# Kernel optimization log

Measured on AMD Instinct MI355X. Metric: run time of the kernel, lower is better.

Reference implementation:

```python
import jax, jax.numpy as jnp
import numpy as np

N = 100000       # nodes
E = 1200000      # edges
D_IN = 64
D_OUT = 64
ALPHA = 0.01     # LeakyReLU negative slope
EPS = 1e-5       # BatchNorm eps


def setup_inputs() -> dict:
    key = jax.random.key(0)
    k0, k1, k2, k3 = jax.random.split(key, 4)
    x = jax.random.normal(k0, (N, D_IN), dtype=jnp.float32)
    edge_idx = jax.random.randint(k1, (2, E), 0, N)
    edge_attr = jax.random.uniform(k2, (E,), dtype=jnp.float32)
    W = jax.random.normal(k3, (D_IN, D_OUT), dtype=jnp.float32) * (1.0 / np.sqrt(D_IN))
    b = jnp.zeros((D_OUT,), dtype=jnp.float32)
    gamma = jnp.ones((D_OUT,), dtype=jnp.float32)
    beta = jnp.zeros((D_OUT,), dtype=jnp.float32)
    return {"x": x, "edge_idx": edge_idx, "edge_attr": edge_attr,
            "W": W, "b": b, "gamma": gamma, "beta": beta}


def reference(x, edge_idx, edge_attr, W, b, gamma, beta):
    n = x.shape[0]
    row, col = edge_idx[0], edge_idx[1]
    # --- GCNConv: add self-loops, symmetric normalization ---
    loops = jnp.arange(n)
    row_f = jnp.concatenate([row, loops])                       # [E+N]
    col_f = jnp.concatenate([col, loops])                       # [E+N]
    w_f = jnp.concatenate([edge_attr, jnp.ones((n,), x.dtype)])  # [E+N]
    deg = jax.ops.segment_sum(w_f, col_f, num_segments=n)       # [N]
    deg_safe = jnp.where(deg > 0, deg, 1.0)
    dis = jnp.where(deg > 0, jax.lax.rsqrt(deg_safe), 0.0)      # deg^-1/2
    norm = dis[row_f] * w_f * dis[col_f]                        # [E+N]
    h = x @ W                                                   # [N, D_OUT]
    msg = norm[:, None] * h[row_f]                              # gather + scale
    agg = jax.ops.segment_sum(msg, col_f, num_segments=n) + b   # scatter-add
    # --- BatchNorm (training-mode batch stats, biased var) ---
    mean = jnp.mean(agg, axis=0)
    var = jnp.mean((agg - mean) ** 2, axis=0)
    hn = (agg - mean) * jax.lax.rsqrt(var + EPS) * gamma + beta
    # --- LeakyReLU ---
    return jnp.where(hn >= 0, hn, ALPHA * hn)
```

## Files before the change

kernel.cpp:

```cpp
#include <hip/hip_runtime.h>

#define D 64
#define ALPHA 0.01f
#define EPS 1e-5f
#define NREP 8
#define CAP 48
#define GSZ 128
#define GMAX 1024
#define NB 512
#define CHUNK 2368
#define BT 512

typedef __attribute__((ext_vector_type(8))) short short8;
typedef __attribute__((ext_vector_type(4))) float f32x4;

__device__ inline unsigned short f2bf(float f) {
    unsigned u = __float_as_uint(f);
    u += 0x7fffu + ((u >> 16) & 1u);
    return (unsigned short)(u >> 16);
}
__device__ inline float bf2f(unsigned short h) { return __uint_as_float((unsigned)h << 16); }

__global__ __launch_bounds__(BT) void k_prepbin(const float4* __restrict__ x4,
                                                ushort4* __restrict__ xb4,
                                                float* __restrict__ stats,
                                                const int* __restrict__ eidx,
                                                const float* __restrict__ w,
                                                uint2* __restrict__ seg,
                                                unsigned short* __restrict__ off16,
                                                long long n16, int G, int E, int chunk) {
    __shared__ uint2 rec[CHUNK];
    __shared__ int h[GMAX + 2];
    __shared__ int ls[BT];
    if (blockIdx.x < NB) {
        int b = blockIdx.x, t = threadIdx.x;
        int e0 = b * chunk;
        int e1 = e0 + chunk; if (e1 > E) e1 = E;
        for (int i = t; i < GMAX + 2; i += BT) h[i] = 0;
        __syncthreads();
        for (int e = e0 + t; e < e1; e += BT) {
            int row = eidx[e];
            int c = eidx[E + e];
            unsigned wq = (unsigned)(w[e] * 32767.0f + 0.5f);
            rec[e - e0] = make_uint2((wq << 17) | (unsigned)row, (unsigned)c);
            atomicAdd(&h[c >> 7], 1);
        }
        __syncthreads();
        int i0 = 2 * t, i1 = 2 * t + 1;
        int a0 = h[i0];
        int a1 = h[i1];
        ls[t] = a0 + a1;
        __syncthreads();
        int own = ls[t];
        for (int off = 1; off < BT; off <<= 1) {
            int v = (t >= off) ? ls[t - off] : 0;
            __syncthreads();
            ls[t] += v;
            __syncthreads();
        }
        int excl = ls[t] - own;
        __syncthreads();
        h[i0] = excl;
        h[i1] = excl + a0;
        __syncthreads();
        unsigned short* ob = off16 + (size_t)b * (G + 1);
        for (int g = t; g <= G; g += BT) ob[g] = (unsigned short)h[g];
        __syncthreads();
        for (int e = e0 + t; e < e1; e += BT) {
            uint2 rv = rec[e - e0];
            int c = (int)rv.y;
            int slot = atomicAdd(&h[c >> 7], 1);
            seg[e0 + slot] = make_uint2(rv.x, (unsigned)(c & (GSZ - 1)));
        }
    } else {
        long long i = (long long)(blockIdx.x - NB) * BT + threadIdx.x;
        if (i < n16) {
            float4 v = x4[i];
            ushort4 r;
            r.x = f2bf(v.x); r.y = f2bf(v.y); r.z = f2bf(v.z); r.w = f2bf(v.w);
            xb4[i] = r;
        }
        if (i < NREP * 128) stats[i] = 0.0f;
    }
}

__global__ __launch_bounds__(BT) void k_binC2(const uint2* __restrict__ seg,
                                              const unsigned short* __restrict__ off16,
                                              unsigned* __restrict__ bucket,
                                              int* __restrict__ cnt,
                                              float* __restrict__ dis,
                                              float* __restrict__ dis_s,
                                              int G, int chunk, int n) {
    __shared__ int cl[GSZ];
    __shared__ float ws[GSZ];
    int g = blockIdx.x;
    if (threadIdx.x < GSZ) { cl[threadIdx.x] = 0; ws[threadIdx.x] = 0.0f; }
    __syncthreads();
    int b = threadIdx.x;
    const unsigned short* ob = off16 + (size_t)b * (G + 1);
    int s = ob[g], e = ob[g + 1];
    size_t base = (size_t)b * chunk;
    for (int i = s; i < e; ++i) {
        uint2 ev = seg[base + i];
        int cig = (int)ev.y;
        int rank = atomicAdd(&cl[cig], 1);
        atomicAdd(&ws[cig], (float)(ev.x >> 17) * (1.0f / 32767.0f));
        int node = g * GSZ + cig;
        if (rank < CAP) bucket[(size_t)node * CAP + rank] = ev.x;
    }
    __syncthreads();
    if (threadIdx.x < GSZ) {
        int node = g * GSZ + threadIdx.x;
        if (node < n) {
            cnt[node] = cl[threadIdx.x];
            float d = rsqrtf(1.0f + ws[threadIdx.x]);
            dis[node] = d;
            dis_s[node] = d * (1.0f / 32767.0f);
        }
    }
}

__global__ __launch_bounds__(256) void k_gather(const unsigned short* __restrict__ xb,
                                                const unsigned* __restrict__ bucket,
                                                const int* __restrict__ cnt,
                                                const float* __restrict__ dis,
                                                const float* __restrict__ dis_s,
                                                unsigned short* __restrict__ aggb, int n) {
    int node = blockIdx.x * 4 + (threadIdx.x >> 6);
    if (node >= n) return;
    int lane = threadIdx.x & 63;
    int g = lane >> 3;
    int l = lane & 7;
    int c = cnt[node];
    if (c > CAP) c = CAP;
    float di = dis[node];
    float acc[8] = {0, 0, 0, 0, 0, 0, 0, 0};
    if (g == 0) {
        short8 xv = *(const short8*)(xb + ((size_t)node << 6) + l * 8);
#pragma unroll
        for (int k = 0; k < 8; ++k) acc[k] = bf2f((unsigned short)xv[k]) * di;
    }
    const unsigned* bkt = bucket + (size_t)node * CAP;
    int j0 = g, j1 = g + 8;
    unsigned v0 = (j0 < c) ? bkt[j0] : 0u;
    unsigned v1 = (j1 < c) ? bkt[j1] : 0u;
    while (j0 < c) {
        int p0 = j0 + 16, p1 = j1 + 16;
        unsigned w0 = (p0 < c) ? bkt[p0] : 0u;
        unsigned w1 = (p1 < c) ? bkt[p1] : 0u;
        int s0 = (int)(v0 & 0x1FFFFu);
        int s1 = (int)(v1 & 0x1FFFFu);
        float nr0 = (float)(v0 >> 17) * dis_s[s0];
        float nr1 = (float)(v1 >> 17) * dis_s[s1];
        short8 x0 = *(const short8*)(xb + ((size_t)s0 << 6) + l * 8);
        short8 x1 = *(const short8*)(xb + ((size_t)s1 << 6) + l * 8);
#pragma unroll
        for (int k = 0; k < 8; ++k) acc[k] += nr0 * bf2f((unsigned short)x0[k]);
#pragma unroll
        for (int k = 0; k < 8; ++k) acc[k] += nr1 * bf2f((unsigned short)x1[k]);
        v0 = w0; v1 = w1; j0 = p0; j1 = p1;
    }
#pragma unroll
    for (int off = 8; off <= 32; off <<= 1)
#pragma unroll
        for (int k = 0; k < 8; ++k) acc[k] += __shfl_xor(acc[k], off, 64);
    if (g == 0) {
        short8 r;
#pragma unroll
        for (int k = 0; k < 8; ++k) r[k] = (short)f2bf(acc[k] * di);
        *(short8*)(aggb + ((size_t)node << 6) + l * 8) = r;
    }
}

__global__ __launch_bounds__(256) void k_gemmstats(const unsigned short* __restrict__ aggb,
                                                   const float* __restrict__ Wm,
                                                   float* __restrict__ stats, int n) {
    __shared__ unsigned short Wt[64 * 64];
    __shared__ float ssum[4][64], qsum[4][64];
    int tid = threadIdx.x;
    for (int i = tid; i < 4096; i += 256) {
        int k = i >> 6, nn = i & 63;
        Wt[nn * 64 + k] = f2bf(Wm[i]);
    }
    __syncthreads();
    int wv = tid >> 6;
    int lane = tid & 63;
    int l15 = lane & 15;
    int quad = lane >> 4;

    short8 bfrag[2][4];
#pragma unroll
    for (int h = 0; h < 2; ++h)
#pragma unroll
        for (int g = 0; g < 4; ++g)
            bfrag[h][g] = *(const short8*)&Wt[(g * 16 + l15) * 64 + h * 32 + quad * 8];

    float s[4] = {0, 0, 0, 0}, q[4] = {0, 0, 0, 0};
    int nwt = (n + 15) >> 4;
    for (int wt = blockIdx.x * 4 + wv; wt < nwt; wt += gridDim.x * 4) {
        int row0 = wt * 16;
        int arow = row0 + l15;
        if (arow >= n) arow = n - 1;
        const unsigned short* ap = aggb + (size_t)arow * 64 + quad * 8;
        short8 a0 = *(const short8*)ap;
        short8 a1 = *(const short8*)(ap + 32);
        f32x4 acc[4] = {{0, 0, 0, 0}, {0, 0, 0, 0}, {0, 0, 0, 0}, {0, 0, 0, 0}};
#pragma unroll
        for (int g = 0; g < 4; ++g) {
            acc[g] = __builtin_amdgcn_mfma_f32_16x16x32_bf16(a0, bfrag[0][g], acc[g], 0, 0, 0);
            acc[g] = __builtin_amdgcn_mfma_f32_16x16x32_bf16(a1, bfrag[1][g], acc[g], 0, 0, 0);
        }
#pragma unroll
        for (int r = 0; r < 4; ++r) {
            int row = row0 + quad * 4 + r;
            if (row < n) {
#pragma unroll
                for (int g = 0; g < 4; ++g) {
                    float v = acc[g][r];
                    s[g] += v;
                    q[g] += v * v;
                }
            }
        }
    }
#pragma unroll
    for (int off = 16; off <= 32; off <<= 1) {
#pragma unroll
        for (int g = 0; g < 4; ++g) {
            s[g] += __shfl_xor(s[g], off, 64);
            q[g] += __shfl_xor(q[g], off, 64);
        }
    }
    if (quad == 0) {
#pragma unroll
        for (int g = 0; g < 4; ++g) { ssum[wv][g * 16 + l15] = s[g]; qsum[wv][g * 16 + l15] = q[g]; }
    }
    __syncthreads();
    float* st = stats + (blockIdx.x & (NREP - 1)) * 128;
    if (tid < 64)
        atomicAdd(&st[tid], ssum[0][tid] + ssum[1][tid] + ssum[2][tid] + ssum[3][tid]);
    else if (tid < 128) {
        int t = tid - 64;
        atomicAdd(&st[64 + t], qsum[0][t] + qsum[1][t] + qsum[2][t] + qsum[3][t]);
    }
}

__global__ __launch_bounds__(256) void k_gemmbn(const unsigned short* __restrict__ aggb,
                                                const float* __restrict__ Wm,
                                                float* __restrict__ out,
                                                const float* __restrict__ stats,
                                                const float* __restrict__ gamma,
                                                const float* __restrict__ beta, int n) {
    __shared__ unsigned short Wt[64 * 64];
    __shared__ float scale[64], shift[64];
    int tid = threadIdx.x;
    for (int i = tid; i < 4096; i += 256) {
        int k = i >> 6, nn = i & 63;
        Wt[nn * 64 + k] = f2bf(Wm[i]);
    }
    if (tid < 64) {
        float sm = 0.0f, qm = 0.0f;
#pragma unroll
        for (int r = 0; r < NREP; ++r) {
            sm += stats[r * 128 + tid];
            qm += stats[r * 128 + 64 + tid];
        }
        float inv_n = 1.0f / (float)n;
        float mean = sm * inv_n;
        float var = qm * inv_n - mean * mean;
        float sc = rsqrtf(var + EPS) * gamma[tid];
        scale[tid] = sc;
        shift[tid] = beta[tid] - mean * sc;
    }
    __syncthreads();
    int wv = tid >> 6;
    int lane = tid & 63;
    int l15 = lane & 15;
    int quad = lane >> 4;

    short8 bfrag[2][4];
    float bsc[4], bsh[4];
#pragma unroll
    for (int h = 0; h < 2; ++h)
#pragma unroll
        for (int g = 0; g < 4; ++g)
            bfrag[h][g] = *(const short8*)&Wt[(g * 16 + l15) * 64 + h * 32 + quad * 8];
#pragma unroll
    for (int g = 0; g < 4; ++g) { bsc[g] = scale[g * 16 + l15]; bsh[g] = shift[g * 16 + l15]; }

    int nwt = (n + 15) >> 4;
    for (int wt = blockIdx.x * 4 + wv; wt < nwt; wt += gridDim.x * 4) {
        int row0 = wt * 16;
        int arow = row0 + l15;
        if (arow >= n) arow = n - 1;
        const unsigned short* ap = aggb + (size_t)arow * 64 + quad * 8;
        short8 a0 = *(const short8*)ap;
        short8 a1 = *(const short8*)(ap + 32);
        f32x4 acc[4] = {{0, 0, 0, 0}, {0, 0, 0, 0}, {0, 0, 0, 0}, {0, 0, 0, 0}};
#pragma unroll
        for (int g = 0; g < 4; ++g) {
            acc[g] = __builtin_amdgcn_mfma_f32_16x16x32_bf16(a0, bfrag[0][g], acc[g], 0, 0, 0);
            acc[g] = __builtin_amdgcn_mfma_f32_16x16x32_bf16(a1, bfrag[1][g], acc[g], 0, 0, 0);
        }
#pragma unroll
        for (int r = 0; r < 4; ++r) {
            int row = row0 + quad * 4 + r;
            if (row < n) {
                size_t base = (size_t)row * 64;
#pragma unroll
                for (int g = 0; g < 4; ++g) {
                    float v = acc[g][r] * bsc[g] + bsh[g];
                    v = v >= 0.0f ? v : ALPHA * v;
                    out[base + g * 16 + l15] = v;
                }
            }
        }
    }
}

extern "C" void kernel_launch(void* const* d_in, const int* in_sizes, int n_in,
                              void* d_out, int out_size, void* d_ws, size_t ws_size,
                              hipStream_t stream) {
    const float* x     = (const float*)d_in[0];
    const int*   eidx  = (const int*)d_in[1];
    const float* eattr = (const float*)d_in[2];
    const float* Wm    = (const float*)d_in[3];
    const float* gamma = (const float*)d_in[5];
    const float* beta  = (const float*)d_in[6];
    float* out = (float*)d_out;

    int n = in_sizes[0] / D;
    int E = in_sizes[2];
    int G = (n + GSZ - 1) / GSZ;
    int chunk = (E + NB - 1) / NB;

    char* p = (char*)d_ws;
    uint2* seg = (uint2*)p;                     p += (size_t)E * 8;
    unsigned* bucket = (unsigned*)p;            p += (size_t)n * CAP * 4;
    unsigned short* xb   = (unsigned short*)p;  p += (size_t)n * D * 2;
    unsigned short* aggb = (unsigned short*)p;  p += (size_t)n * D * 2;
    int* cnt = (int*)p;                         p += (size_t)n * 4;
    float* dis = (float*)p;                     p += (size_t)n * 4;
    float* dis_s = (float*)p;                   p += (size_t)n * 4;
    float* stats = (float*)p;                   p += NREP * 128 * 4;
    unsigned short* off16 = (unsigned short*)p; p += (((size_t)NB * (G + 1) * 2 + 15) & ~15ULL);

    long long n16 = (long long)n * 16;
    unsigned prep_blocks = (unsigned)((n16 + BT - 1) / BT);

    k_prepbin<<<NB + prep_blocks, BT, 0, stream>>>(
        (const float4*)x, (ushort4*)xb, stats, eidx, eattr, seg, off16, n16, G, E, chunk);
    k_binC2<<<G, BT, 0, stream>>>(seg, off16, bucket, cnt, dis, dis_s, G, chunk, n);
    k_gather<<<(n + 3) / 4, 256, 0, stream>>>(xb, bucket, cnt, dis, dis_s, aggb, n);
    k_gemmstats<<<1024, 256, 0, stream>>>(aggb, Wm, stats, n);
    k_gemmbn<<<1024, 256, 0, stream>>>(aggb, Wm, out, stats, gamma, beta, n);
}
```

Measured before the change: 181.9 us.

## Fuse GEMM-stats and GEMM-BN kernels with a grid barrier and register-held tiles

Merges the two GEMM passes into one persistent kernel of 512 blocks. Each wave computes up to four 16-row tiles, keeps the results in registers, and accumulates the BatchNorm statistics. A global atomic counter then acts as a grid-wide barrier, after which the kept tiles are normalized and written out. This removes the second read of aggb, the repeated GEMM and one kernel launch. In exchange it relies on all 512 blocks being co-resident to avoid deadlock, and it raises register pressure.

```diff
diff --git a/kernel.cpp b/kernel.cpp
--- a/kernel.cpp
+++ b/kernel.cpp
@@ -10,6 +10,7 @@
 #define NB 512
 #define CHUNK 2368
 #define BT 512
+#define GF_BLOCKS 512
 
 typedef __attribute__((ext_vector_type(8))) short short8;
 typedef __attribute__((ext_vector_type(4))) float f32x4;
@@ -24,6 +25,7 @@
 __global__ __launch_bounds__(BT) void k_prepbin(const float4* __restrict__ x4,
                                                 ushort4* __restrict__ xb4,
                                                 float* __restrict__ stats,
+                                                int* __restrict__ done,
                                                 const int* __restrict__ eidx,
                                                 const float* __restrict__ w,
                                                 uint2* __restrict__ seg,
@@ -81,6 +83,7 @@
             xb4[i] = r;
         }
         if (i < NREP * 128) stats[i] = 0.0f;
+        if (i == 0) *done = 0;
     }
 }
 
@@ -172,98 +175,100 @@
     }
 }
 
-__global__ __launch_bounds__(256) void k_gemmstats(const unsigned short* __restrict__ aggb,
-                                                   const float* __restrict__ Wm,
-                                                   float* __restrict__ stats, int n) {
+__global__ __launch_bounds__(256, 2) void k_gemmfused(const unsigned short* __restrict__ aggb,
+                                                      const float* __restrict__ Wm,
+                                                      float* __restrict__ out,
+                                                      float* __restrict__ stats,
+                                                      const float* __restrict__ gamma,
+                                                      const float* __restrict__ beta,
+                                                      int* __restrict__ done, int n) {
     __shared__ unsigned short Wt[64 * 64];
     __shared__ float ssum[4][64], qsum[4][64];
-    int tid = threadIdx.x;
-    for (int i = tid; i < 4096; i += 256) {
-        int k = i >> 6, nn = i & 63;
-        Wt[nn * 64 + k] = f2bf(Wm[i]);
-    }
-    __syncthreads();
-    int wv = tid >> 6;
-    int lane = tid & 63;
-    int l15 = lane & 15;
-    int quad = lane >> 4;
-
-    short8 bfrag[2][4];
-#pragma unroll
-    for (int h = 0; h < 2; ++h)
-#pragma unroll
-        for (int g = 0; g < 4; ++g)
-            bfrag[h][g] = *(const short8*)&Wt[(g * 16 + l15) * 64 + h * 32 + quad * 8];
-
-    float s[4] = {0, 0, 0, 0}, q[4] = {0, 0, 0, 0};
-    int nwt = (n + 15) >> 4;
-    for (int wt = blockIdx.x * 4 + wv; wt < nwt; wt += gridDim.x * 4) {
-        int row0 = wt * 16;
-        int arow = row0 + l15;
-        if (arow >= n) arow = n - 1;
-        const unsigned short* ap = aggb + (size_t)arow * 64 + quad * 8;
-        short8 a0 = *(const short8*)ap;
-        short8 a1 = *(const short8*)(ap + 32);
-        f32x4 acc[4] = {{0, 0, 0, 0}, {0, 0, 0, 0}, {0, 0, 0, 0}, {0, 0, 0, 0}};
-#pragma unroll
-        for (int g = 0; g < 4; ++g) {
-            acc[g] = __builtin_amdgcn_mfma_f32_16x16x32_bf16(a0, bfrag[0][g], acc[g], 0, 0, 0);
-            acc[g] = __builtin_amdgcn_mfma_f32_16x16x32_bf16(a1, bfrag[1][g], acc[g], 0, 0, 0);
-        }
-#pragma unroll
-        for (int r = 0; r < 4; ++r) {
-            int row = row0 + quad * 4 + r;
-            if (row < n) {
-#pragma unroll
-                for (int g = 0; g < 4; ++g) {
-                    float v = acc[g][r];
-                    s[g] += v;
-                    q[g] += v * v;
-                }
-            }
-        }
-    }
-#pragma unroll
-    for (int off = 16; off <= 32; off <<= 1) {
-#pragma unroll
-        for (int g = 0; g < 4; ++g) {
-            s[g] += __shfl_xor(s[g], off, 64);
-            q[g] += __shfl_xor(q[g], off, 64);
-        }
-    }
-    if (quad == 0) {
-#pragma unroll
-        for (int g = 0; g < 4; ++g) { ssum[wv][g * 16 + l15] = s[g]; qsum[wv][g * 16 + l15] = q[g]; }
-    }
-    __syncthreads();
-    float* st = stats + (blockIdx.x & (NREP - 1)) * 128;
-    if (tid < 64)
-        atomicAdd(&st[tid], ssum[0][tid] + ssum[1][tid] + ssum[2][tid] + ssum[3][tid]);
-    else if (tid < 128) {
-        int t = tid - 64;
-        atomicAdd(&st[64 + t], qsum[0][t] + qsum[1][t] + qsum[2][t] + qsum[3][t]);
-    }
-}
-
-__global__ __launch_bounds__(256) void k_gemmbn(const unsigned short* __restrict__ aggb,
-                                                const float* __restrict__ Wm,
-                                                float* __restrict__ out,
-                                                const float* __restrict__ stats,
-                                                const float* __restrict__ gamma,
-                                                const float* __restrict__ beta, int n) {
-    __shared__ unsigned short Wt[64 * 64];
     __shared__ float scale[64], shift[64];
     int tid = threadIdx.x;
     for (int i = tid; i < 4096; i += 256) {
         int k = i >> 6, nn = i & 63;
         Wt[nn * 64 + k] = f2bf(Wm[i]);
     }
+    __syncthreads();
+    int wv = tid >> 6;
+    int lane = tid & 63;
+    int l15 = lane & 15;
+    int quad = lane >> 4;
+
+    short8 bfrag[2][4];
+#pragma unroll
+    for (int h = 0; h < 2; ++h)
+#pragma unroll
+        for (int g = 0; g < 4; ++g)
+            bfrag[h][g] = *(const short8*)&Wt[(g * 16 + l15) * 64 + h * 32 + quad * 8];
+
+    int nwt = (n + 15) >> 4;
+    int wvg = blockIdx.x * 4 + wv;
+    const int WST = GF_BLOCKS * 4;
+
+    float s[4] = {0, 0, 0, 0}, q[4] = {0, 0, 0, 0};
+    f32x4 acc[4][4];
+
+#pragma unroll
+    for (int t = 0; t < 4; ++t) {
+        int wt = wvg + t * WST;
+        if (wt < nwt) {
+            int row0 = wt * 16;
+            int arow = row0 + l15;
+            if (arow >= n) arow = n - 1;
+            const unsigned short* ap = aggb + (size_t)arow * 64 + quad * 8;
+            short8 a0 = *(const short8*)ap;
+            short8 a1 = *(const short8*)(ap + 32);
+#pragma unroll
+            for (int g = 0; g < 4; ++g) {
+                f32x4 z = {0, 0, 0, 0};
+                z = __builtin_amdgcn_mfma_f32_16x16x32_bf16(a0, bfrag[0][g], z, 0, 0, 0);
+                z = __builtin_amdgcn_mfma_f32_16x16x32_bf16(a1, bfrag[1][g], z, 0, 0, 0);
+                acc[t][g] = z;
+#pragma unroll
+                for (int r = 0; r < 4; ++r) {
+                    int row = row0 + quad * 4 + r;
+                    if (row < n) { float v = z[r]; s[g] += v; q[g] += v * v; }
+                }
+            }
+        }
+    }
+#pragma unroll
+    for (int off = 16; off <= 32; off <<= 1) {
+#pragma unroll
+        for (int g = 0; g < 4; ++g) {
+            s[g] += __shfl_xor(s[g], off, 64);
+            q[g] += __shfl_xor(q[g], off, 64);
+        }
+    }
+    if (quad == 0) {
+#pragma unroll
+        for (int g = 0; g < 4; ++g) { ssum[wv][g * 16 + l15] = s[g]; qsum[wv][g * 16 + l15] = q[g]; }
+    }
+    __syncthreads();
+    float* st = stats + (blockIdx.x & (NREP - 1)) * 128;
+    if (tid < 64)
+        atomicAdd(&st[tid], ssum[0][tid] + ssum[1][tid] + ssum[2][tid] + ssum[3][tid]);
+    else if (tid < 128) {
+        int t2 = tid - 64;
+        atomicAdd(&st[64 + t2], qsum[0][t2] + qsum[1][t2] + qsum[2][t2] + qsum[3][t2]);
+    }
+    __syncthreads();
+
+    if (tid == 0) {
+        __threadfence();
+        atomicAdd(done, 1);
+        while (__hip_atomic_load(done, __ATOMIC_ACQUIRE, __HIP_MEMORY_SCOPE_AGENT) < GF_BLOCKS) {}
+    }
+    __syncthreads();
+
     if (tid < 64) {
         float sm = 0.0f, qm = 0.0f;
 #pragma unroll
         for (int r = 0; r < NREP; ++r) {
-            sm += stats[r * 128 + tid];
-            qm += stats[r * 128 + 64 + tid];
+            sm += __hip_atomic_load(&stats[r * 128 + tid], __ATOMIC_RELAXED, __HIP_MEMORY_SCOPE_AGENT);
+            qm += __hip_atomic_load(&stats[r * 128 + 64 + tid], __ATOMIC_RELAXED, __HIP_MEMORY_SCOPE_AGENT);
         }
         float inv_n = 1.0f / (float)n;
         float mean = sm * inv_n;
@@ -273,45 +278,24 @@
         shift[tid] = beta[tid] - mean * sc;
     }
     __syncthreads();
-    int wv = tid >> 6;
-    int lane = tid & 63;
-    int l15 = lane & 15;
-    int quad = lane >> 4;
-
-    short8 bfrag[2][4];
-    float bsc[4], bsh[4];
-#pragma unroll
-    for (int h = 0; h < 2; ++h)
-#pragma unroll
-        for (int g = 0; g < 4; ++g)
-            bfrag[h][g] = *(const short8*)&Wt[(g * 16 + l15) * 64 + h * 32 + quad * 8];
-#pragma unroll
-    for (int g = 0; g < 4; ++g) { bsc[g] = scale[g * 16 + l15]; bsh[g] = shift[g * 16 + l15]; }
-
-    int nwt = (n + 15) >> 4;
-    for (int wt = blockIdx.x * 4 + wv; wt < nwt; wt += gridDim.x * 4) {
-        int row0 = wt * 16;
-        int arow = row0 + l15;
-        if (arow >= n) arow = n - 1;
-        const unsigned short* ap = aggb + (size_t)arow * 64 + quad * 8;
-        short8 a0 = *(const short8*)ap;
-        short8 a1 = *(const short8*)(ap + 32);
-        f32x4 acc[4] = {{0, 0, 0, 0}, {0, 0, 0, 0}, {0, 0, 0, 0}, {0, 0, 0, 0}};
-#pragma unroll
-        for (int g = 0; g < 4; ++g) {
-            acc[g] = __builtin_amdgcn_mfma_f32_16x16x32_bf16(a0, bfrag[0][g], acc[g], 0, 0, 0);
-            acc[g] = __builtin_amdgcn_mfma_f32_16x16x32_bf16(a1, bfrag[1][g], acc[g], 0, 0, 0);
-        }
-#pragma unroll
-        for (int r = 0; r < 4; ++r) {
-            int row = row0 + quad * 4 + r;
-            if (row < n) {
-                size_t base = (size_t)row * 64;
-#pragma unroll
-                for (int g = 0; g < 4; ++g) {
-                    float v = acc[g][r] * bsc[g] + bsh[g];
-                    v = v >= 0.0f ? v : ALPHA * v;
-                    out[base + g * 16 + l15] = v;
+
+#pragma unroll
+    for (int t = 0; t < 4; ++t) {
+        int wt = wvg + t * WST;
+        if (wt < nwt) {
+            int row0 = wt * 16;
+#pragma unroll
+            for (int g = 0; g < 4; ++g) {
+                float sc = scale[g * 16 + l15];
+                float sh = shift[g * 16 + l15];
+#pragma unroll
+                for (int r = 0; r < 4; ++r) {
+                    int row = row0 + quad * 4 + r;
+                    if (row < n) {
+                        float v = acc[t][g][r] * sc + sh;
+                        v = v >= 0.0f ? v : ALPHA * v;
+                        out[(size_t)row * 64 + g * 16 + l15] = v;
+                    }
                 }
             }
         }
@@ -343,15 +327,15 @@
     float* dis = (float*)p;                     p += (size_t)n * 4;
     float* dis_s = (float*)p;                   p += (size_t)n * 4;
     float* stats = (float*)p;                   p += NREP * 128 * 4;
+    int* done = (int*)p;                        p += 16;
     unsigned short* off16 = (unsigned short*)p; p += (((size_t)NB * (G + 1) * 2 + 15) & ~15ULL);
 
     long long n16 = (long long)n * 16;
     unsigned prep_blocks = (unsigned)((n16 + BT - 1) / BT);
 
     k_prepbin<<<NB + prep_blocks, BT, 0, stream>>>(
-        (const float4*)x, (ushort4*)xb, stats, eidx, eattr, seg, off16, n16, G, E, chunk);
+        (const float4*)x, (ushort4*)xb, stats, done, eidx, eattr, seg, off16, n16, G, E, chunk);
     k_binC2<<<G, BT, 0, stream>>>(seg, off16, bucket, cnt, dis, dis_s, G, chunk, n);
     k_gather<<<(n + 3) / 4, 256, 0, stream>>>(xb, bucket, cnt, dis, dis_s, aggb, n);
-    k_gemmstats<<<1024, 256, 0, stream>>>(aggb, Wm, stats, n);
-    k_gemmbn<<<1024, 256, 0, stream>>>(aggb, Wm, out, stats, gamma, beta, n);
-}
+    k_gemmfused<<<GF_BLOCKS, 256, 0, stream>>>(aggb, Wm, out, stats, gamma, beta, done, n);
+}
```

New measurement: 218.3 us. 1.2x slower.
